# Performance work log

Measured on AMD Instinct MI355X. Metric: run time of the kernel, lower is better.

The kernel has to match this reference:

```python
import jax, jax.numpy as jnp
import numpy as np

B, N, D = 32, 128, 64
E = N * N
EPS = 1e-5


def _bn(x, gamma, beta):
    # torch BatchNorm1d on (B, C, D): normalize per-channel over (batch, last dim)
    mean = jnp.mean(x, axis=(0, 2), keepdims=True)
    var = jnp.var(x, axis=(0, 2), keepdims=True)
    return (x - mean) * jax.lax.rsqrt(var + EPS) * gamma[None, :, None] + beta[None, :, None]


def _gat_layer(x, edge, Wh, We, Wp, Wa, gv, bv, ge, be):
    b, n, d = x.shape
    res = x
    z_h = jnp.einsum('bnd,od->bno', x, Wh)   # fc_h (torch Linear: y = x W^T)
    z_e = jnp.einsum('bed,od->beo', edge, We)  # fc_e
    # incidence matmuls are pure gathers: edge e = i*n + j
    z_src = jnp.broadcast_to(z_h[:, None, :, :], (b, n, n, d)).reshape(b, n * n, d)  # start: edge (i,j) <- node j
    z_dst = jnp.broadcast_to(z_h[:, :, None, :], (b, n, n, d)).reshape(b, n * n, d)  # end:   edge (i,j) <- node i
    z = jnp.concatenate([z_src, z_dst, z_e], axis=-1)  # (b, E, 3d)
    z_e_new = jnp.einsum('bec,oc->beo', z, Wp)  # fc_proj
    attn = jnp.einsum('bec,c->be', z, Wa[0])    # attn_fc -> (b, E)
    attn = jnp.where(attn >= 0, attn, 0.01 * attn)  # LeakyReLU(0.01)
    attn = jax.nn.softmax(attn.reshape(b, n, n), axis=2).reshape(b, n * n)  # softmax over sources j
    # scatter via end^T: node i <- sum_j attn[i,j] * z_src[i*n+j]
    agg = (attn[:, :, None] * z_src).reshape(b, n, n, d).sum(axis=2)
    x_new = jax.nn.elu(res + _bn(agg, gv, bv))
    edge_new = jax.nn.elu(_bn(z_e_new, ge, be))
    return x_new, edge_new


def setup_inputs():
    key = jax.random.key(0)
    ks = jax.random.split(key, 10)
    scale = float(np.sqrt(2.0 / D))
    return {
        'x': jax.random.normal(ks[0], (B, N, D), jnp.float32),
        'edge': jax.random.normal(ks[1], (B, E, D), jnp.float32),
        'Wh1': jax.random.normal(ks[2], (D, D), jnp.float32) * scale,
        'We1': jax.random.normal(ks[3], (D, D), jnp.float32) * scale,
        'Wp1': jax.random.normal(ks[4], (D, 3 * D), jnp.float32) * scale,
        'Wa1': jax.random.normal(ks[5], (1, 3 * D), jnp.float32) * scale,
        'Wh2': jax.random.normal(ks[6], (D, D), jnp.float32) * scale,
        'We2': jax.random.normal(ks[7], (D, D), jnp.float32) * scale,
        'Wp2': jax.random.normal(ks[8], (D, 3 * D), jnp.float32) * scale,
        'Wa2': jax.random.normal(ks[9], (1, 3 * D), jnp.float32) * scale,
        'gv1': jnp.ones((N,), jnp.float32), 'bv1': jnp.zeros((N,), jnp.float32),
        'ge1': jnp.ones((E,), jnp.float32), 'be1': jnp.zeros((E,), jnp.float32),
        'gv2': jnp.ones((N,), jnp.float32), 'bv2': jnp.zeros((N,), jnp.float32),
        'ge2': jnp.ones((E,), jnp.float32), 'be2': jnp.zeros((E,), jnp.float32),
    }


def reference(x, edge, Wh1, We1, Wp1, Wa1, Wh2, We2, Wp2, Wa2,
              gv1, bv1, ge1, be1, gv2, bv2, ge2, be2):
    x, edge = _gat_layer(x, edge, Wh1, We1, Wp1, Wa1, gv1, bv1, ge1, be1)
    x, edge = _gat_layer(x, edge, Wh2, We2, Wp2, Wa2, gv2, bv2, ge2, be2)
    return x, edge
```

## Files before the change

### kernel.cpp

```cpp
#include <hip/hip_runtime.h>
#include <math.h>

#define BB 32
#define NN 128
#define DD 64
#define EE (NN*NN)
#define EPSI 1e-5f

typedef __attribute__((ext_vector_type(8))) short bf16x8;
typedef __attribute__((ext_vector_type(4))) float f32x4;

__device__ __forceinline__ short f2bf(float f) {
    union { float f; unsigned u; } v; v.f = f;
    unsigned u = v.u;
    unsigned r = (u + 0x7FFFu + ((u >> 16) & 1u)) >> 16;
    return (short)r;
}
__device__ __forceinline__ float elu(float v) {
    return v > 0.f ? v : __expf(v) - 1.f;
}

__global__ void k_fold(const float* __restrict__ Wp, const float* __restrict__ We,
                       const float* __restrict__ Wa,
                       short* __restrict__ Mbf, short* __restrict__ wbf)
{
    int t = blockIdx.x * 256 + threadIdx.x;
    int d = t >> 6, k = t & 63;
    float acc = 0.f;
    for (int o = 0; o < DD; ++o)
        acc += Wp[d*192 + 128 + o] * We[o*DD + k];
    Mbf[d*DD + k] = f2bf(acc);
    if (d == 0) {
        float aw = 0.f;
        for (int o = 0; o < DD; ++o)
            aw += Wa[128 + o] * We[o*DD + k];
        wbf[k] = f2bf(aw);
    }
}

__global__ void k_node(const float* __restrict__ x, const float* __restrict__ Wh,
                       const float* __restrict__ Wp, const float* __restrict__ Wa,
                       float* __restrict__ zh, float* __restrict__ PsT,
                       float* __restrict__ PdT, float* __restrict__ sO,
                       float* __restrict__ tO)
{
    int row = blockIdx.x;
    int b = row >> 7, n = row & 127;
    int d = threadIdx.x;
    __shared__ float xr[DD];
    __shared__ float zr[DD];
    xr[d] = x[row*DD + d];
    __syncthreads();
    float acc = 0.f;
#pragma unroll
    for (int k = 0; k < DD; ++k) acc += xr[k] * Wh[d*DD + k];
    zr[d] = acc;
    zh[row*DD + d] = acc;
    __syncthreads();
    float a0 = 0.f, a1 = 0.f;
#pragma unroll
    for (int o = 0; o < DD; ++o) {
        float z = zr[o];
        a0 += Wp[d*192 + o]      * z;
        a1 += Wp[d*192 + 64 + o] * z;
    }
    const int fi = ((b >> 4)*4 + (d >> 4))*256 + (((b >> 2) & 3)*16 + (d & 15))*4 + (b & 3);
    PsT[n*2048 + fi] = a0;
    PdT[n*2048 + fi] = a1;
    float sv = zr[d] * Wa[d];
    float tv = zr[d] * Wa[64 + d];
#pragma unroll
    for (int off = 32; off; off >>= 1) {
        sv += __shfl_xor(sv, off);
        tv += __shfl_xor(tv, off);
    }
    if (d == 0) { sO[row] = sv; tO[row] = tv; }
}

template <int INM, int OUTM>
__global__ __launch_bounds__(256, 4) void k_edge(
    const void* __restrict__ einv,
    const short* __restrict__ Mbf,
    const short* __restrict__ wbf,
    const float* __restrict__ PsT,
    const float* __restrict__ PdT,
    const float* __restrict__ ge, const float* __restrict__ be,
    void* __restrict__ eoutv, float* __restrict__ uout)
{
    __shared__ float zl[4][16][68];
    const int l  = threadIdx.x & 63;
    const int wv = threadIdx.x >> 6;
    const int lr = l & 15;
    const int lg = l >> 4;
    const int e  = blockIdx.x * 4 + wv;
    const int i0 = e >> 7, j0 = e & 127;
    float (*Z)[68] = zl[wv];

    bf16x8 afr[2][2];
    if constexpr (INM == 0) {
        const float* ein = (const float*)einv;
#pragma unroll
        for (int m = 0; m < 2; ++m) {
            const float* rowp = ein + ((size_t)(16*m + lr)*EE + e)*DD;
            const float4 v0 = *reinterpret_cast<const float4*>(rowp +      lg*8);
            const float4 v1 = *reinterpret_cast<const float4*>(rowp +      lg*8 + 4);
            const float4 v2 = *reinterpret_cast<const float4*>(rowp + 32 + lg*8);
            const float4 v3 = *reinterpret_cast<const float4*>(rowp + 32 + lg*8 + 4);
            afr[m][0][0]=f2bf(v0.x); afr[m][0][1]=f2bf(v0.y); afr[m][0][2]=f2bf(v0.z); afr[m][0][3]=f2bf(v0.w);
            afr[m][0][4]=f2bf(v1.x); afr[m][0][5]=f2bf(v1.y); afr[m][0][6]=f2bf(v1.z); afr[m][0][7]=f2bf(v1.w);
            afr[m][1][0]=f2bf(v2.x); afr[m][1][1]=f2bf(v2.y); afr[m][1][2]=f2bf(v2.z); afr[m][1][3]=f2bf(v2.w);
            afr[m][1][4]=f2bf(v3.x); afr[m][1][5]=f2bf(v3.y); afr[m][1][6]=f2bf(v3.z); afr[m][1][7]=f2bf(v3.w);
        }
    } else {
        const short* ein = (const short*)einv + (size_t)e*BB*DD;
#pragma unroll
        for (int m = 0; m < 2; ++m)
#pragma unroll
            for (int s = 0; s < 2; ++s)
                afr[m][s] = *reinterpret_cast<const bf16x8*>(ein + (16*m + lr)*DD + s*32 + lg*8);
    }

    bf16x8 bfr[4][2];
#pragma unroll
    for (int n = 0; n < 4; ++n)
#pragma unroll
        for (int s = 0; s < 2; ++s)
            bfr[n][s] = *reinterpret_cast<const bf16x8*>(Mbf + (16*n + lr)*DD + s*32 + lg*8);
    const bf16x8 zerov = (bf16x8){0,0,0,0,0,0,0,0};
    bf16x8 wfrag[2];
#pragma unroll
    for (int s = 0; s < 2; ++s)
        wfrag[s] = (lr == 0) ? *reinterpret_cast<const bf16x8*>(wbf + s*32 + lg*8) : zerov;

    f32x4 acc[2][4];
    f32x4 uacc[2];
    {
        const float* psb = PsT + j0*2048;
        const float* pdb = PdT + i0*2048;
#pragma unroll
        for (int m = 0; m < 2; ++m) {
            uacc[m] = (f32x4){0.f, 0.f, 0.f, 0.f};
#pragma unroll
            for (int n = 0; n < 4; ++n) {
                const float4 a = *reinterpret_cast<const float4*>(psb + (m*4+n)*256 + l*4);
                const float4 c = *reinterpret_cast<const float4*>(pdb + (m*4+n)*256 + l*4);
                acc[m][n] = (f32x4){a.x+c.x, a.y+c.y, a.z+c.z, a.w+c.w};
            }
        }
    }

#pragma unroll
    for (int m = 0; m < 2; ++m) {
#pragma unroll
        for (int n = 0; n < 4; ++n)
            acc[m][n] = __builtin_amdgcn_mfma_f32_16x16x32_bf16(afr[m][0], bfr[n][0], acc[m][n], 0, 0, 0);
        uacc[m] = __builtin_amdgcn_mfma_f32_16x16x32_bf16(afr[m][0], wfrag[0], uacc[m], 0, 0, 0);
#pragma unroll
        for (int n = 0; n < 4; ++n)
            acc[m][n] = __builtin_amdgcn_mfma_f32_16x16x32_bf16(afr[m][1], bfr[n][1], acc[m][n], 0, 0, 0);
        uacc[m] = __builtin_amdgcn_mfma_f32_16x16x32_bf16(afr[m][1], wfrag[1], uacc[m], 0, 0, 0);
    }

    float s1 = 0.f, s2 = 0.f;
#pragma unroll
    for (int m = 0; m < 2; ++m)
#pragma unroll
        for (int n = 0; n < 4; ++n)
#pragma unroll
            for (int q = 0; q < 4; ++q) { float v = acc[m][n][q]; s1 += v; s2 += v*v; }
#pragma unroll
    for (int off = 1; off < 64; off <<= 1) {
        s1 += __shfl_xor(s1, off);
        s2 += __shfl_xor(s2, off);
    }
    const float mean = s1 * (1.f/2048.f);
    const float var  = s2 * (1.f/2048.f) - mean*mean;
    const float sc = ge[e] * rsqrtf(var + EPSI);
    const float sh = be[e] - mean*sc;

#pragma unroll
    for (int m = 0; m < 2; ++m)
#pragma unroll
        for (int n = 0; n < 4; ++n)
#pragma unroll
            for (int q = 0; q < 4; ++q)
                acc[m][n][q] = elu(acc[m][n][q]*sc + sh);

    if (lr == 0) {
#pragma unroll
        for (int m = 0; m < 2; ++m)
#pragma unroll
            for (int q = 0; q < 4; ++q)
                uout[(size_t)(16*m + 4*lg + q)*EE + e] = uacc[m][q];
    }

#pragma unroll
    for (int h = 0; h < 2; ++h) {
#pragma unroll
        for (int n = 0; n < 4; ++n)
#pragma unroll
            for (int q = 0; q < 4; ++q)
                Z[4*lg + q][16*n + lr] = acc[h][n][q];
        __builtin_amdgcn_s_waitcnt(0);
        if constexpr (OUTM == 0) {
            float* eout = (float*)eoutv;
#pragma unroll
            for (int it = 0; it < 4; ++it) {
                const int rr = lg + 4*it;
                const int b  = 16*h + rr;
                float4 z = *reinterpret_cast<float4*>(&Z[rr][lr*4]);
                *reinterpret_cast<float4*>(eout + ((size_t)b*EE + e)*DD + lr*4) = z;
            }
        } else {
            short* eout = (short*)eoutv + (size_t)e*BB*DD;
#pragma unroll
            for (int it = 0; it < 2; ++it) {
                const int rr = (l >> 3) + 8*it;
                const int b  = 16*h + rr;
                const int c0 = (l & 7)*8;
                float4 zlo = *reinterpret_cast<float4*>(&Z[rr][c0]);
                float4 zhi = *reinterpret_cast<float4*>(&Z[rr][c0+4]);
                bf16x8 o;
                o[0]=f2bf(zlo.x); o[1]=f2bf(zlo.y); o[2]=f2bf(zlo.z); o[3]=f2bf(zlo.w);
                o[4]=f2bf(zhi.x); o[5]=f2bf(zhi.y); o[6]=f2bf(zhi.z); o[7]=f2bf(zhi.w);
                *reinterpret_cast<bf16x8*>(eout + b*DD + c0) = o;
            }
        }
        __builtin_amdgcn_s_waitcnt(0);
    }
}

__global__ void k_attn(const float* __restrict__ sI, const float* __restrict__ tI,
                       const float* __restrict__ u, const float* __restrict__ zh,
                       float* __restrict__ agg)
{
    int blk = blockIdx.x; int b = blk >> 7, i = blk & 127;
    int l = threadIdx.x;
    __shared__ float at[NN];
    float ti = tI[blk];
    float l0 = sI[b*NN + l]      + ti + u[b*EE + i*NN + l];
    float l1 = sI[b*NN + l + 64] + ti + u[b*EE + i*NN + l + 64];
    l0 = l0 >= 0.f ? l0 : 0.01f*l0;
    l1 = l1 >= 0.f ? l1 : 0.01f*l1;
    float mx = fmaxf(l0, l1);
#pragma unroll
    for (int off = 32; off; off >>= 1) mx = fmaxf(mx, __shfl_xor(mx, off));
    float e0 = __expf(l0 - mx), e1 = __expf(l1 - mx);
    float sm = e0 + e1;
#pragma unroll
    for (int off = 32; off; off >>= 1) sm += __shfl_xor(sm, off);
    float inv = 1.f / sm;
    at[l]      = e0 * inv;
    at[l + 64] = e1 * inv;
    __syncthreads();
    float acc = 0.f;
    for (int j = 0; j < NN; ++j) acc += at[j] * zh[(b*NN + j)*DD + l];
    agg[(b*NN + i)*DD + l] = acc;
}

__global__ void k_vbn(const float* __restrict__ agg, const float* __restrict__ xres,
                      const float* __restrict__ gv, const float* __restrict__ bv,
                      float* __restrict__ xout)
{
    int i = blockIdx.x, t = threadIdx.x;
    float vals[8];
    float s1 = 0.f, s2 = 0.f;
#pragma unroll
    for (int q = 0; q < 8; ++q) {
        int m = t + 256*q; int b = m >> 6, d = m & 63;
        float v = agg[(b*NN + i)*DD + d];
        vals[q] = v; s1 += v; s2 += v*v;
    }
#pragma unroll
    for (int off = 1; off < 64; off <<= 1) {
        s1 += __shfl_xor(s1, off);
        s2 += __shfl_xor(s2, off);
    }
    __shared__ float r1[4], r2[4];
    int wv = t >> 6;
    if ((t & 63) == 0) { r1[wv] = s1; r2[wv] = s2; }
    __syncthreads();
    s1 = r1[0] + r1[1] + r1[2] + r1[3];
    s2 = r2[0] + r2[1] + r2[2] + r2[3];
    float mean  = s1 * (1.f/2048.f);
    float var   = s2 * (1.f/2048.f) - mean*mean;
    float scale = gv[i] * rsqrtf(var + EPSI);
    float shift = bv[i] - mean*scale;
#pragma unroll
    for (int q = 0; q < 8; ++q) {
        int m = t + 256*q; int b = m >> 6, d = m & 63;
        float v = vals[q]*scale + shift + xres[(b*NN + i)*DD + d];
        xout[(b*NN + i)*DD + d] = v > 0.f ? v : __expf(v) - 1.f;
    }
}

extern "C" void kernel_launch(void* const* d_in, const int* in_sizes, int n_in,
                              void* d_out, int out_size, void* d_ws, size_t ws_size,
                              hipStream_t stream)
{
    const float* x    = (const float*)d_in[0];
    const float* edge = (const float*)d_in[1];
    const float* Wh1  = (const float*)d_in[2];
    const float* We1  = (const float*)d_in[3];
    const float* Wp1  = (const float*)d_in[4];
    const float* Wa1  = (const float*)d_in[5];
    const float* Wh2  = (const float*)d_in[6];
    const float* We2  = (const float*)d_in[7];
    const float* Wp2  = (const float*)d_in[8];
    const float* Wa2  = (const float*)d_in[9];
    const float* gv1  = (const float*)d_in[10];
    const float* bv1  = (const float*)d_in[11];
    const float* ge1  = (const float*)d_in[12];
    const float* be1  = (const float*)d_in[13];
    const float* gv2  = (const float*)d_in[14];
    const float* bv2  = (const float*)d_in[15];
    const float* ge2  = (const float*)d_in[16];
    const float* be2  = (const float*)d_in[17];

    float* xout = (float*)d_out;
    float* eout = (float*)d_out + BB*NN*DD;

    float* ws  = (float*)d_ws;
    short* Mbf = (short*)ws;  ws += DD*DD/2;
    short* wbf = (short*)ws;  ws += DD/2;
    float* zh  = ws;  ws += BB*NN*DD;
    float* PsT = ws;  ws += NN*BB*DD;
    float* PdT = ws;  ws += NN*BB*DD;
    float* sb  = ws;  ws += BB*NN;
    float* tb  = ws;  ws += BB*NN;
    float* ub  = ws;  ws += BB*EE;
    float* agg = ws;  ws += BB*NN*DD;
    float* x1  = ws;  ws += BB*NN*DD;
    short* e1bf = (short*)ws;
    const size_t need = ((size_t)(ws - (float*)d_ws))*4 + (size_t)EE*BB*DD*2;

    const bool dense = (ws_size >= need);

    k_fold<<<16, 256, 0, stream>>>(Wp1, We1, Wa1, Mbf, wbf);
    k_node<<<BB*NN, 64, 0, stream>>>(x, Wh1, Wp1, Wa1, zh, PsT, PdT, sb, tb);
    if (dense)
        k_edge<0,1><<<EE/4, 256, 0, stream>>>(edge, Mbf, wbf, PsT, PdT, ge1, be1, e1bf, ub);
    else
        k_edge<0,0><<<EE/4, 256, 0, stream>>>(edge, Mbf, wbf, PsT, PdT, ge1, be1, eout, ub);
    k_attn<<<BB*NN, 64, 0, stream>>>(sb, tb, ub, zh, agg);
    k_vbn<<<NN, 256, 0, stream>>>(agg, x, gv1, bv1, x1);
    k_fold<<<16, 256, 0, stream>>>(Wp2, We2, Wa2, Mbf, wbf);
    k_node<<<BB*NN, 64, 0, stream>>>(x1, Wh2, Wp2, Wa2, zh, PsT, PdT, sb, tb);
    if (dense)
        k_edge<1,0><<<EE/4, 256, 0, stream>>>(e1bf, Mbf, wbf, PsT, PdT, ge2, be2, eout, ub);
    else
        k_edge<0,0><<<EE/4, 256, 0, stream>>>(eout, Mbf, wbf, PsT, PdT, ge2, be2, eout, ub);
    k_attn<<<BB*NN, 64, 0, stream>>>(sb, tb, ub, zh, agg);
    k_vbn<<<NN, 256, 0, stream>>>(agg, x1, gv2, bv2, xout);
}
```

Baseline: 217.3 us.

## Stage fp32 edge input via block-cooperative coalesced loads into LDS

For the fp32 input path of the edge kernel, the four waves now cooperatively load the block's four contiguous edge rows per batch as float4s, convert them to bf16, and stage them in a shared LDS buffer before reading MFMA fragments. Previously each lane read scattered 32-byte chunks directly from global memory. The LDS buffer is reused as the output transpose scratch, and the full waitcnt(0) barriers are narrowed to lgkmcnt(0) so outstanding global stores no longer stall the wave. In exchange it adds a block-wide __syncthreads and relies on the reused LDS region being large enough for the float scratch.

New measurement: 208.6 us. 4.0% less time.

```diff
diff --git a/kernel.cpp b/kernel.cpp
--- a/kernel.cpp
+++ b/kernel.cpp
@@ -8,7 +8,11 @@
 #define EPSI 1e-5f
 
 typedef __attribute__((ext_vector_type(8))) short bf16x8;
+typedef __attribute__((ext_vector_type(4))) short s16x4;
 typedef __attribute__((ext_vector_type(4))) float f32x4;
+
+#define LGKM0() do { asm volatile("s_waitcnt lgkmcnt(0)" ::: "memory"); \
+                     __builtin_amdgcn_sched_barrier(0); } while (0)
 
 __device__ __forceinline__ short f2bf(float f) {
     union { float f; unsigned u; } v; v.f = f;
@@ -87,37 +91,51 @@
     const float* __restrict__ ge, const float* __restrict__ be,
     void* __restrict__ eoutv, float* __restrict__ uout)
 {
-    __shared__ float zl[4][16][68];
-    const int l  = threadIdx.x & 63;
-    const int wv = threadIdx.x >> 6;
+    __shared__ short As[4][32][72];
+    const int t  = threadIdx.x;
+    const int l  = t & 63;
+    const int wv = t >> 6;
     const int lr = l & 15;
     const int lg = l >> 4;
-    const int e  = blockIdx.x * 4 + wv;
+    const int e0 = blockIdx.x * 4;
+    const int e  = e0 + wv;
     const int i0 = e >> 7, j0 = e & 127;
-    float (*Z)[68] = zl[wv];
 
     bf16x8 afr[2][2];
     if constexpr (INM == 0) {
         const float* ein = (const float*)einv;
-#pragma unroll
-        for (int m = 0; m < 2; ++m) {
-            const float* rowp = ein + ((size_t)(16*m + lr)*EE + e)*DD;
-            const float4 v0 = *reinterpret_cast<const float4*>(rowp +      lg*8);
-            const float4 v1 = *reinterpret_cast<const float4*>(rowp +      lg*8 + 4);
-            const float4 v2 = *reinterpret_cast<const float4*>(rowp + 32 + lg*8);
-            const float4 v3 = *reinterpret_cast<const float4*>(rowp + 32 + lg*8 + 4);
-            afr[m][0][0]=f2bf(v0.x); afr[m][0][1]=f2bf(v0.y); afr[m][0][2]=f2bf(v0.z); afr[m][0][3]=f2bf(v0.w);
-            afr[m][0][4]=f2bf(v1.x); afr[m][0][5]=f2bf(v1.y); afr[m][0][6]=f2bf(v1.z); afr[m][0][7]=f2bf(v1.w);
-            afr[m][1][0]=f2bf(v2.x); afr[m][1][1]=f2bf(v2.y); afr[m][1][2]=f2bf(v2.z); afr[m][1][3]=f2bf(v2.w);
-            afr[m][1][4]=f2bf(v3.x); afr[m][1][5]=f2bf(v3.y); afr[m][1][6]=f2bf(v3.z); afr[m][1][7]=f2bf(v3.w);
+        const int tq = (t >> 4) & 3;
+        const int d0 = (t & 15) * 4;
+        float4 sv[8];
+#pragma unroll
+        for (int it = 0; it < 8; ++it) {
+            const int b = it*4 + wv;
+            sv[it] = *reinterpret_cast<const float4*>(
+                         ein + ((size_t)b*EE + e0 + tq)*DD + d0);
         }
+#pragma unroll
+        for (int it = 0; it < 8; ++it) {
+            const int b = it*4 + wv;
+            s16x4 o;
+            o[0] = f2bf(sv[it].x); o[1] = f2bf(sv[it].y);
+            o[2] = f2bf(sv[it].z); o[3] = f2bf(sv[it].w);
+            *reinterpret_cast<s16x4*>(&As[tq][b][d0]) = o;
+        }
+        __syncthreads();
+#pragma unroll
+        for (int m = 0; m < 2; ++m)
+#pragma unroll
+            for (int s = 0; s < 2; ++s)
+                afr[m][s] = *reinterpret_cast<const bf16x8*>(
+                                &As[wv][16*m + lr][s*32 + lg*8]);
     } else {
         const short* ein = (const short*)einv + (size_t)e*BB*DD;
 #pragma unroll
         for (int m = 0; m < 2; ++m)
 #pragma unroll
             for (int s = 0; s < 2; ++s)
-                afr[m][s] = *reinterpret_cast<const bf16x8*>(ein + (16*m + lr)*DD + s*32 + lg*8);
+                afr[m][s] = *reinterpret_cast<const bf16x8*>(
+                                ein + (16*m + lr)*DD + s*32 + lg*8);
     }
 
     bf16x8 bfr[4][2];
@@ -194,6 +212,8 @@
                 uout[(size_t)(16*m + 4*lg + q)*EE + e] = uacc[m][q];
     }
 
+    float (*Z)[68] = reinterpret_cast<float (*)[68]>(&As[wv][0][0]);
+    LGKM0();
 #pragma unroll
     for (int h = 0; h < 2; ++h) {
 #pragma unroll
@@ -201,7 +221,7 @@
 #pragma unroll
             for (int q = 0; q < 4; ++q)
                 Z[4*lg + q][16*n + lr] = acc[h][n][q];
-        __builtin_amdgcn_s_waitcnt(0);
+        LGKM0();
         if constexpr (OUTM == 0) {
             float* eout = (float*)eoutv;
 #pragma unroll
@@ -226,7 +246,7 @@
                 *reinterpret_cast<bf16x8*>(eout + b*DD + c0) = o;
             }
         }
-        __builtin_amdgcn_s_waitcnt(0);
+        LGKM0();
     }
 }
 
```
